# Performance work log

Measured on AMD Instinct MI355X. Metric: run time of the kernel, lower is better.

Reference implementation:

```python
import jax, jax.numpy as jnp
import numpy as np


def setup_inputs() -> dict:
    key = jax.random.key(0)
    ks = jax.random.split(key, 13)
    B, T, C = 256, 80, 512
    H = 512
    NC = 6625
    S = 25
    s = 0.02
    inp = {
        "inputs": jax.random.normal(ks[0], (B, T, C), jnp.float32),
        "targets": jax.random.randint(ks[1], (B, S), 0, NC),
        "batch_max_length": S,
        "i2h_w": jax.random.normal(ks[2], (H, C), jnp.float32) * s,
        "h2h_w": jax.random.normal(ks[3], (H, H), jnp.float32) * s,
        "h2h_b": jax.random.normal(ks[4], (H,), jnp.float32) * s,
        "score_w": jax.random.normal(ks[5], (1, H), jnp.float32) * s,
        "gru_wih": jax.random.normal(ks[6], (3 * H, C + NC), jnp.float32) * s,
        "gru_whh": jax.random.normal(ks[7], (3 * H, H), jnp.float32) * s,
        "gru_bih": jax.random.normal(ks[8], (3 * H,), jnp.float32) * s,
        "gru_bhh": jax.random.normal(ks[9], (3 * H,), jnp.float32) * s,
        "gen_w": jax.random.normal(ks[10], (NC, H), jnp.float32) * s,
        "gen_b": jax.random.normal(ks[11], (NC,), jnp.float32) * s,
    }
    return inp


def reference(inputs, targets, batch_max_length, i2h_w, h2h_w, h2h_b, score_w,
              gru_wih, gru_whh, gru_bih, gru_bhh, gen_w, gen_b):
    B, T, C = inputs.shape
    H = h2h_w.shape[0]
    NC = gen_w.shape[0]
    S = batch_max_length

    # i2h has no bias; same result every step, hoisted out of the loop
    batch_H_proj = inputs @ i2h_w.T  # [B, T, H]
    # teacher-forcing one-hots for all steps: [S, B, NC]
    onehots = jax.nn.one_hot(targets.T, NC, dtype=inputs.dtype)

    def gru_cell(x, h):
        gi = x @ gru_wih.T + gru_bih  # [B, 3H]
        gh = h @ gru_whh.T + gru_bhh  # [B, 3H]
        i_r, i_z, i_n = jnp.split(gi, 3, axis=1)
        h_r, h_z, h_n = jnp.split(gh, 3, axis=1)
        r = jax.nn.sigmoid(i_r + h_r)
        z = jax.nn.sigmoid(i_z + h_z)
        n = jnp.tanh(i_n + r * h_n)
        return (1.0 - z) * n + z * h

    def step(h, onehot_t):
        prev_proj = h @ h2h_w.T + h2h_b  # [B, H]
        res = jnp.tanh(batch_H_proj + prev_proj[:, None, :])  # [B, T, H]
        e = jnp.einsum('bth,h->bt', res, score_w[0])  # [B, T]
        alpha = jax.nn.softmax(e, axis=1)
        context = jnp.einsum('bt,btc->bc', alpha, inputs)  # [B, C]
        x = jnp.concatenate([context, onehot_t], axis=1)  # [B, C+NC]
        h_new = gru_cell(x, h)
        return h_new, h_new

    h0 = jnp.zeros((B, H), inputs.dtype)
    _, hiddens = jax.lax.scan(step, h0, onehots)  # [S, B, H]
    output = jnp.transpose(hiddens, (1, 0, 2))  # [B, S, H]
    probs = output @ gen_w.T + gen_b  # [B, S, NC] (training path: no softmax)
    return probs
```

## Files before the change

kernel.cpp:

```cpp
#include <hip/hip_runtime.h>
#include <stdint.h>

typedef float f32x4 __attribute__((ext_vector_type(4)));
typedef int i32x4 __attribute__((ext_vector_type(4)));

#define LOG2E 1.4426950408889634f

__device__ __forceinline__ float bf2f(unsigned short u) {
  union { unsigned int i; float f; } x; x.i = ((unsigned int)u) << 16; return x.f;
}
__device__ __forceinline__ float bfu_lo(unsigned u) {
  union { unsigned int i; float f; } x; x.i = u << 16; return x.f;
}
__device__ __forceinline__ float bfu_hi(unsigned u) {
  union { unsigned int i; float f; } x; x.i = u & 0xffff0000u; return x.f;
}
__device__ __forceinline__ unsigned short f2bf(float f) {
  union { float f; unsigned int i; } x; x.f = f;
  unsigned int u = x.i + 0x7fffu + ((x.i >> 16) & 1u);
  return (unsigned short)(u >> 16);
}
__device__ __forceinline__ float fexp2(float x) {
#if __has_builtin(__builtin_amdgcn_exp2f)
  return __builtin_amdgcn_exp2f(x);
#else
  return exp2f(x);
#endif
}
__device__ __forceinline__ float frcp(float x) {
#if __has_builtin(__builtin_amdgcn_rcpf)
  return __builtin_amdgcn_rcpf(x);
#else
  return 1.f / x;
#endif
}
__device__ __forceinline__ float fast_exp(float x) { return fexp2(x * LOG2E); }
__device__ __forceinline__ float fast_tanh(float x) {
  float e = fexp2(x * (2.f * LOG2E));
  return 1.f - 2.f * frcp(e + 1.f);
}
__device__ __forceinline__ float fast_sigmoid(float x) {
  return frcp(1.f + fexp2(-x * LOG2E));
}

__device__ __forceinline__ void mfma_bf16_16x16x32(f32x4& d, i32x4 a, i32x4 b) {
  asm("v_mfma_f32_16x16x32_bf16 %0, %1, %2, %0" : "+v"(d) : "v"(a), "v"(b));
}

__device__ __forceinline__ void stage16(const unsigned short* g, unsigned short* lds_wave_base, int lane) {
#if __has_builtin(__builtin_amdgcn_global_load_lds)
  __builtin_amdgcn_global_load_lds(
      (const __attribute__((address_space(1))) unsigned int*)(uintptr_t)g,
      (__attribute__((address_space(3))) unsigned int*)(uintptr_t)lds_wave_base,
      16, 0, 0);
#else
  i32x4 v = *(const i32x4*)g;
  *(i32x4*)(lds_wave_base + lane * 8) = v;
#endif
}

__device__ __forceinline__ void xcd_swizzle(int& bx, int& by) {
  int nx = gridDim.x, nwg = nx * gridDim.y;
  if ((nwg & 7) == 0) {
    int id = by * nx + bx;
    int q = nwg >> 3;
    int swz = (id & 7) * q + (id >> 3);
    bx = swz % nx;
    by = swz / nx;
  }
}

#define BM 128
#define BN 128
#define BK 32

template <bool OUT_BF16, bool BIAS>
__device__ __forceinline__ void gemm_body(
    const unsigned short* __restrict__ A, const unsigned short* __restrict__ B,
    void* __restrict__ Cout, const float* __restrict__ bias,
    int K, int ldc, int nbound, int m0, int n0)
{
  __shared__ __align__(16) unsigned short lA[BM * BK];
  __shared__ __align__(16) unsigned short lB[BN * BK];
  const int tid = threadIdx.x;
  const int lane = tid & 63;
  const int w = tid >> 6;
  const int wm = w >> 1, wn = w & 1;
  const int frag_row = lane & 15;
  const int kgrp = lane >> 4;

  f32x4 acc[4][4];
#pragma unroll
  for (int i = 0; i < 4; ++i)
#pragma unroll
    for (int j = 0; j < 4; ++j) acc[i][j] = 0.f;

  const int nK = K / BK;
  const int c0 = tid, c1 = tid + 256;
  for (int kt = 0; kt < nK; ++kt) {
    const int kb = kt * BK;
    stage16(A + (size_t)(m0 + (c0 >> 2)) * K + kb + (c0 & 3) * 8, lA + (w * 64) * 8, lane);
    stage16(A + (size_t)(m0 + (c1 >> 2)) * K + kb + (c1 & 3) * 8, lA + (256 + w * 64) * 8, lane);
    stage16(B + (size_t)(n0 + (c0 >> 2)) * K + kb + (c0 & 3) * 8, lB + (w * 64) * 8, lane);
    stage16(B + (size_t)(n0 + (c1 >> 2)) * K + kb + (c1 & 3) * 8, lB + (256 + w * 64) * 8, lane);
    __syncthreads();

    i32x4 af[4], bfr[4];
#pragma unroll
    for (int i = 0; i < 4; ++i) {
      int ra = wm * 64 + i * 16 + frag_row;
      af[i] = *(const i32x4*)&lA[ra * BK + kgrp * 8];
      int rb = wn * 64 + i * 16 + frag_row;
      bfr[i] = *(const i32x4*)&lB[rb * BK + kgrp * 8];
    }
#pragma unroll
    for (int i = 0; i < 4; ++i)
#pragma unroll
      for (int j = 0; j < 4; ++j) mfma_bf16_16x16x32(acc[i][j], af[i], bfr[j]);
    __syncthreads();
  }

  const int crow = (lane >> 4) * 4;
  const int ccol = lane & 15;
#pragma unroll
  for (int i = 0; i < 4; ++i) {
#pragma unroll
    for (int j = 0; j < 4; ++j) {
      int gn = n0 + wn * 64 + j * 16 + ccol;
      if (gn < nbound) {
        float bv = BIAS ? bias[gn] : 0.f;
        int gmb = m0 + wm * 64 + i * 16 + crow;
#pragma unroll
        for (int r = 0; r < 4; ++r) {
          float v = acc[i][j][r] + bv;
          if (OUT_BF16) ((unsigned short*)Cout)[(size_t)(gmb + r) * ldc + gn] = f2bf(v);
          else          ((float*)Cout)[(size_t)(gmb + r) * ldc + gn] = v;
        }
      }
    }
  }
}

__global__ __launch_bounds__(256) void gemm_bf16out_kernel(
    const unsigned short* __restrict__ A, const unsigned short* __restrict__ B,
    unsigned short* __restrict__ C, int K, int ldc) {
  int bx = blockIdx.x, by = blockIdx.y;
  xcd_swizzle(bx, by);
  gemm_body<true, false>(A, B, C, nullptr, K, ldc, 1 << 30, by * BM, bx * BN);
}
__global__ __launch_bounds__(256) void gemm_f32bias_kernel(
    const unsigned short* __restrict__ A, const unsigned short* __restrict__ B,
    float* __restrict__ C, const float* __restrict__ bias, int K, int ldc, int nbound) {
  int bx = blockIdx.x, by = blockIdx.y;
  xcd_swizzle(bx, by);
  gemm_body<false, true>(A, B, C, bias, K, ldc, nbound, by * BM, bx * BN);
}

__global__ __launch_bounds__(256) void cast_bf16_kernel(
    const float* __restrict__ src, unsigned short* __restrict__ dst, int n4) {
  int i = blockIdx.x * 256 + threadIdx.x;
  if (i < n4) {
    float4 v = ((const float4*)src)[i];
    ushort4 o;
    o.x = f2bf(v.x); o.y = f2bf(v.y); o.z = f2bf(v.z); o.w = f2bf(v.w);
    ((ushort4*)dst)[i] = o;
  }
}
__global__ __launch_bounds__(256) void cast_wihc_kernel(
    const float* __restrict__ wih, unsigned short* __restrict__ dst) {
  int i = blockIdx.x * 256 + threadIdx.x;
  int j = i >> 9, c = i & 511;
  dst[i] = f2bf(wih[(size_t)j * 7137 + c]);
}
__global__ __launch_bounds__(256) void pack_h2h_kernel(
    const float* __restrict__ src, unsigned short* __restrict__ dst) {
  int i = blockIdx.x * 256 + threadIdx.x;
  int row = i >> 9, c = i & 511;
  int kb = c >> 3, kk = c & 7;
  dst[((size_t)kb * 512 + row) * 8 + kk] = f2bf(src[i]);
}
__global__ __launch_bounds__(256) void cast_genw_kernel(
    const float* __restrict__ g, unsigned short* __restrict__ dst) {
  int i = blockIdx.x * 256 + threadIdx.x;
  if (i < 6656 * 512) {
    int nrow = i >> 9, c = i & 511;
    float v = (nrow < 6625) ? g[(size_t)nrow * 512 + c] : 0.f;
    dst[i] = f2bf(v);
  }
}
__global__ __launch_bounds__(256) void transpose_oh_kernel(
    const float* __restrict__ wih, unsigned short* __restrict__ dst) {
  __shared__ float tile[32][33];
  int t0 = blockIdx.x * 32;
  int j0 = blockIdx.y * 32;
  int c = threadIdx.x & 31;
  int r4 = threadIdx.x >> 5;
#pragma unroll
  for (int rr = 0; rr < 4; ++rr) {
    int r = r4 + rr * 8;
    int tcol = t0 + c;
    tile[r][c] = (tcol < 6625) ? wih[(size_t)(j0 + r) * 7137 + 512 + tcol] : 0.f;
  }
  __syncthreads();
#pragma unroll
  for (int rr = 0; rr < 4; ++rr) {
    int r = r4 + rr * 8;
    int trow = t0 + r;
    if (trow < 6625) dst[(size_t)trow * 1536 + j0 + c] = f2bf(tile[c][r]);
  }
}

__global__ __launch_bounds__(512) void attn_step_kernel(
    const unsigned short* __restrict__ proj_bf,
    const unsigned short* __restrict__ inputs_bf,
    const unsigned short* __restrict__ h2hP,
    const float* __restrict__ h2h_b,
    const float* __restrict__ score_w,
    const unsigned short* __restrict__ h_in,
    unsigned short* __restrict__ ctx_bf,
    int s)
{
  __shared__ float h_lds[512];
  __shared__ float pp_lds[512];
  __shared__ float e_s[80];
  __shared__ float alpha_s[80];

  const int tid = threadIdx.x;
  const int lane = tid & 63;
  const int w = tid >> 6;
  const int b = blockIdx.x;

  if (s > 0) h_lds[tid] = bf2f(h_in[b * 512 + tid]);
  __syncthreads();

  float pacc = h2h_b[tid];
  if (s > 0) {
    const unsigned short* wp = h2hP + (size_t)tid * 8;
#pragma unroll 4
    for (int kb = 0; kb < 64; ++kb) {
      union { i32x4 v; unsigned int u[4]; } wu;
      wu.v = *(const i32x4*)(wp + (size_t)kb * 4096);
#pragma unroll
      for (int q = 0; q < 4; ++q) {
        pacc = fmaf(bfu_lo(wu.u[q]), h_lds[kb * 8 + 2 * q], pacc);
        pacc = fmaf(bfu_hi(wu.u[q]), h_lds[kb * 8 + 2 * q + 1], pacc);
      }
    }
  }
  pp_lds[tid] = pacc;
  __syncthreads();

  float ppv[8], swv[8];
#pragma unroll
  for (int j = 0; j < 8; ++j) ppv[j] = pp_lds[lane * 8 + j];
  *(float4*)&swv[0] = *(const float4*)(score_w + lane * 8);
  *(float4*)&swv[4] = *(const float4*)(score_w + lane * 8 + 4);

  for (int t = w; t < 80; t += 8) {
    union { i32x4 v; unsigned int u[4]; } u;
    u.v = *(const i32x4*)(proj_bf + (size_t)(b * 80 + t) * 512 + lane * 8);
    float acc = 0.f;
#pragma unroll
    for (int q = 0; q < 4; ++q) {
      acc += fast_tanh(bfu_lo(u.u[q]) + ppv[2 * q]) * swv[2 * q];
      acc += fast_tanh(bfu_hi(u.u[q]) + ppv[2 * q + 1]) * swv[2 * q + 1];
    }
#pragma unroll
    for (int m = 32; m >= 1; m >>= 1) acc += __shfl_xor(acc, m, 64);
    if (lane == 0) e_s[t] = acc;
  }
  __syncthreads();
  if (w == 0) {
    float v0 = e_s[lane];
    float v1 = (lane < 16) ? e_s[64 + lane] : -1e30f;
    float mx = fmaxf(v0, v1);
#pragma unroll
    for (int m = 32; m >= 1; m >>= 1) mx = fmaxf(mx, __shfl_xor(mx, m, 64));
    float a0 = fast_exp(v0 - mx);
    float a1 = (lane < 16) ? fast_exp(v1 - mx) : 0.f;
    float sm = a0 + a1;
#pragma unroll
    for (int m = 32; m >= 1; m >>= 1) sm += __shfl_xor(sm, m, 64);
    float inv = frcp(sm);
    alpha_s[lane] = a0 * inv;
    if (lane < 16) alpha_s[64 + lane] = a1 * inv;
  }
  __syncthreads();

  float cacc = 0.f;
  const unsigned short* ip = inputs_bf + (size_t)b * 40960;
#pragma unroll 8
  for (int t = 0; t < 80; ++t)
    cacc = fmaf(alpha_s[t], bf2f(ip[t * 512 + tid]), cacc);
  ctx_bf[(size_t)b * 512 + tid] = f2bf(cacc);
}

__global__ __launch_bounds__(256) void gru_step_kernel(
    const unsigned short* __restrict__ h_in,
    const unsigned short* __restrict__ ctx,
    const unsigned short* __restrict__ whh,
    const unsigned short* __restrict__ wihc,
    const unsigned short* __restrict__ ohT,
    const int* __restrict__ targets,
    const float* __restrict__ bih, const float* __restrict__ bhh,
    unsigned short* __restrict__ h_out,
    unsigned short* __restrict__ hid_bf,
    int s)
{
  __shared__ __align__(16) char sm[49152];
  unsigned short* lAh = (unsigned short*)sm;
  unsigned short* lAc = lAh + 4096;
  unsigned short* lBw = lAh + 8192;
  unsigned short* lBi = lAh + 14336;

  const int tid = threadIdx.x;
  const int lane = tid & 63;
  const int w = tid >> 6;
  const int fr = lane & 15, kg = lane >> 4;
  const int wm = w >> 1, wn = w & 1;
  const int m0 = blockIdx.y * 64;
  const int c0 = blockIdx.x * 32;

  f32x4 ag[2][3], ai[2][3];
#pragma unroll
  for (int i = 0; i < 2; ++i)
#pragma unroll
    for (int j = 0; j < 3; ++j) { ag[i][j] = 0.f; ai[i][j] = 0.f; }

  for (int kt = 0; kt < 8; ++kt) {
    const int kb = kt * 64;
#pragma unroll
    for (int i = 0; i < 2; ++i) {
      int c = tid + i * 256;
      int row = c >> 3, k8 = c & 7;
      int sk8 = k8 ^ (row & 7);
      stage16(h_in + (size_t)(m0 + row) * 512 + kb + sk8 * 8, lAh + (i * 256 + w * 64) * 8, lane);
      stage16(ctx  + (size_t)(m0 + row) * 512 + kb + sk8 * 8, lAc + (i * 256 + w * 64) * 8, lane);
    }
#pragma unroll
    for (int i = 0; i < 3; ++i) {
      int c = tid + i * 256;
      int br = c >> 3, k8 = c & 7;
      int sk8 = k8 ^ (br & 7);
      int gr = (br >> 5) * 512 + c0 + (br & 31);
      stage16(whh  + (size_t)gr * 512 + kb + sk8 * 8, lBw + (i * 256 + w * 64) * 8, lane);
      stage16(wihc + (size_t)gr * 512 + kb + sk8 * 8, lBi + (i * 256 + w * 64) * 8, lane);
    }
    __syncthreads();

#pragma unroll
    for (int ks = 0; ks < 2; ++ks) {
      const int kc = ks * 4 + kg;
      i32x4 ah[2], ac[2], bw[3], bi[3];
#pragma unroll
      for (int i = 0; i < 2; ++i) {
        int r = wm * 32 + i * 16 + fr;
        int off = r * 64 + (kc ^ (r & 7)) * 8;
        ah[i] = *(const i32x4*)&lAh[off];
        ac[i] = *(const i32x4*)&lAc[off];
      }
#pragma unroll
      for (int j = 0; j < 3; ++j) {
        int r = wn * 48 + j * 16 + fr;
        int off = r * 64 + (kc ^ (r & 7)) * 8;
        bw[j] = *(const i32x4*)&lBw[off];
        bi[j] = *(const i32x4*)&lBi[off];
      }
#pragma unroll
      for (int i = 0; i < 2; ++i)
#pragma unroll
        for (int j = 0; j < 3; ++j) {
          mfma_bf16_16x16x32(ag[i][j], ah[i], bw[j]);
          mfma_bf16_16x16x32(ai[i][j], ac[i], bi[j]);
        }
    }
    __syncthreads();
  }

  float* accg = (float*)sm;
  float* acci = accg + 6144;
  const int crow = (lane >> 4) * 4;
  const int ccol = lane & 15;
#pragma unroll
  for (int i = 0; i < 2; ++i)
#pragma unroll
    for (int j = 0; j < 3; ++j) {
      int col = wn * 48 + j * 16 + ccol;
#pragma unroll
      for (int r = 0; r < 4; ++r) {
        int row = wm * 32 + i * 16 + crow + r;
        accg[row * 96 + col] = ag[i][j][r];
        acci[row * 96 + col] = ai[i][j][r];
      }
    }
  __syncthreads();

#pragma unroll
  for (int e = tid; e < 2048; e += 256) {
    int row = e >> 5, cc = e & 31;
    int b = m0 + row, ch = c0 + cc;
    int tgt = targets[b * 25 + s];
    const unsigned short* oh = ohT + (size_t)tgt * 1536;
    float ghr = accg[row * 96 + cc]      + bhh[ch];
    float ghz = accg[row * 96 + 32 + cc] + bhh[512 + ch];
    float ghn = accg[row * 96 + 64 + cc] + bhh[1024 + ch];
    float gir = acci[row * 96 + cc]      + bih[ch]        + bf2f(oh[ch]);
    float giz = acci[row * 96 + 32 + cc] + bih[512 + ch]  + bf2f(oh[512 + ch]);
    float gin = acci[row * 96 + 64 + cc] + bih[1024 + ch] + bf2f(oh[1024 + ch]);
    float r_ = fast_sigmoid(gir + ghr);
    float z_ = fast_sigmoid(giz + ghz);
    float n_ = fast_tanh(gin + r_ * ghn);
    float h = (1.f - z_) * n_ + z_ * bf2f(h_in[(size_t)b * 512 + ch]);
    unsigned short hb = f2bf(h);
    h_out[(size_t)b * 512 + ch] = hb;
    hid_bf[((size_t)b * 25 + s) * 512 + ch] = hb;
  }
}

extern "C" void kernel_launch(void* const* d_in, const int* in_sizes, int n_in,
                              void* d_out, int out_size, void* d_ws, size_t ws_size,
                              hipStream_t stream) {
  (void)in_sizes; (void)n_in; (void)out_size; (void)ws_size;
  const float* inputs  = (const float*)d_in[0];
  const int*   targets = (const int*)d_in[1];
  const float* i2h_w   = (const float*)d_in[3];
  const float* h2h_w   = (const float*)d_in[4];
  const float* h2h_b   = (const float*)d_in[5];
  const float* score_w = (const float*)d_in[6];
  const float* gru_wih = (const float*)d_in[7];
  const float* gru_whh = (const float*)d_in[8];
  const float* gru_bih = (const float*)d_in[9];
  const float* gru_bhh = (const float*)d_in[10];
  const float* gen_w   = (const float*)d_in[11];
  const float* gen_b   = (const float*)d_in[12];
  float* out = (float*)d_out;

  char* ws = (char*)d_ws;
  size_t off = 0;
  auto alloc = [&](size_t bytes) {
    char* p = ws + off;
    off += (bytes + 255) & ~(size_t)255;
    return p;
  };
  unsigned short* inputs_bf = (unsigned short*)alloc(10485760ull * 2);
  unsigned short* proj_bf   = (unsigned short*)alloc(10485760ull * 2);
  unsigned short* i2h_bf    = (unsigned short*)alloc(262144ull * 2);
  unsigned short* h2hP_bf   = (unsigned short*)alloc(262144ull * 2);
  unsigned short* whh_bf    = (unsigned short*)alloc(786432ull * 2);
  unsigned short* wihc_bf   = (unsigned short*)alloc(786432ull * 2);
  unsigned short* ohT_bf    = (unsigned short*)alloc(10176000ull * 2);
  unsigned short* genw_bf   = (unsigned short*)alloc(3407872ull * 2);
  unsigned short* ctx_bf    = (unsigned short*)alloc(131072ull * 2);
  unsigned short* hbuf0     = (unsigned short*)alloc(131072ull * 2);
  unsigned short* hbuf1     = (unsigned short*)alloc(131072ull * 2);
  unsigned short* hid_bf    = (unsigned short*)alloc(3276800ull * 2);

  cast_bf16_kernel<<<10240, 256, 0, stream>>>(inputs, inputs_bf, 2621440);
  cast_bf16_kernel<<<256, 256, 0, stream>>>(i2h_w, i2h_bf, 65536);
  pack_h2h_kernel<<<1024, 256, 0, stream>>>(h2h_w, h2hP_bf);
  cast_bf16_kernel<<<768, 256, 0, stream>>>(gru_whh, whh_bf, 196608);
  cast_wihc_kernel<<<3072, 256, 0, stream>>>(gru_wih, wihc_bf);
  transpose_oh_kernel<<<dim3(208, 48), 256, 0, stream>>>(gru_wih, ohT_bf);
  cast_genw_kernel<<<13312, 256, 0, stream>>>(gen_w, genw_bf);
  gemm_bf16out_kernel<<<dim3(4, 160), 256, 0, stream>>>(inputs_bf, i2h_bf, proj_bf, 512, 512);
  hipMemsetAsync(hbuf0, 0, 131072 * 2, stream);

  unsigned short* hb[2] = {hbuf0, hbuf1};
  for (int s = 0; s < 25; ++s) {
    attn_step_kernel<<<256, 512, 0, stream>>>(
        proj_bf, inputs_bf, h2hP_bf, h2h_b, score_w, hb[s & 1], ctx_bf, s);
    gru_step_kernel<<<dim3(16, 4), 256, 0, stream>>>(
        hb[s & 1], ctx_bf, whh_bf, wihc_bf, ohT_bf, targets,
        gru_bih, gru_bhh, hb[(s + 1) & 1], hid_bf, s);
  }

  gemm_f32bias_kernel<<<dim3(52, 50), 256, 0, stream>>>(hid_bf, genw_bf, out, gen_b, 512, 6625, 6625);
}
```

Measured before the change: 975.4 us.

## Widen GEMM K-tile with XOR-swizzled LDS, generalize XCD swizzle, fuse prep casts

The GEMM K-tile grows from 32 to 64 and LDS staging uses an XOR swizzle on the 16-byte chunk index. This halves the number of barrier-separated K iterations and should cut LDS bank conflicts on fragment reads. The XCD swizzle now also handles grid sizes that are not a multiple of 8, so the 52x50 output GEMM gets remapped too. The seven weight and input cast/pack kernels are merged into one launch to save launch overhead. The cost is more LDS per block, which may lower occupancy.

```diff
diff --git a/kernel.cpp b/kernel.cpp
--- a/kernel.cpp
+++ b/kernel.cpp
@@ -61,18 +61,17 @@
 
 __device__ __forceinline__ void xcd_swizzle(int& bx, int& by) {
   int nx = gridDim.x, nwg = nx * gridDim.y;
-  if ((nwg & 7) == 0) {
-    int id = by * nx + bx;
-    int q = nwg >> 3;
-    int swz = (id & 7) * q + (id >> 3);
-    bx = swz % nx;
-    by = swz / nx;
-  }
+  int id = by * nx + bx;
+  int q = nwg >> 3, r = nwg & 7;
+  int x = id & 7, j = id >> 3;
+  int swz = (x < r ? x * (q + 1) : r * (q + 1) + (x - r) * q) + j;
+  bx = swz % nx;
+  by = swz / nx;
 }
 
 #define BM 128
 #define BN 128
-#define BK 32
+#define BK 64
 
 template <bool OUT_BF16, bool BIAS>
 __device__ __forceinline__ void gemm_body(
@@ -86,8 +85,8 @@
   const int lane = tid & 63;
   const int w = tid >> 6;
   const int wm = w >> 1, wn = w & 1;
-  const int frag_row = lane & 15;
-  const int kgrp = lane >> 4;
+  const int fr = lane & 15;
+  const int kg = lane >> 4;
 
   f32x4 acc[4][4];
 #pragma unroll
@@ -96,27 +95,34 @@
     for (int j = 0; j < 4; ++j) acc[i][j] = 0.f;
 
   const int nK = K / BK;
-  const int c0 = tid, c1 = tid + 256;
   for (int kt = 0; kt < nK; ++kt) {
     const int kb = kt * BK;
-    stage16(A + (size_t)(m0 + (c0 >> 2)) * K + kb + (c0 & 3) * 8, lA + (w * 64) * 8, lane);
-    stage16(A + (size_t)(m0 + (c1 >> 2)) * K + kb + (c1 & 3) * 8, lA + (256 + w * 64) * 8, lane);
-    stage16(B + (size_t)(n0 + (c0 >> 2)) * K + kb + (c0 & 3) * 8, lB + (w * 64) * 8, lane);
-    stage16(B + (size_t)(n0 + (c1 >> 2)) * K + kb + (c1 & 3) * 8, lB + (256 + w * 64) * 8, lane);
+#pragma unroll
+    for (int i = 0; i < 4; ++i) {
+      int c = tid + i * 256;
+      int row = c >> 3, k8 = c & 7;
+      int sk8 = k8 ^ (row & 7);
+      stage16(A + (size_t)(m0 + row) * K + kb + sk8 * 8, lA + (i * 256 + w * 64) * 8, lane);
+      stage16(B + (size_t)(n0 + row) * K + kb + sk8 * 8, lB + (i * 256 + w * 64) * 8, lane);
+    }
     __syncthreads();
 
-    i32x4 af[4], bfr[4];
-#pragma unroll
-    for (int i = 0; i < 4; ++i) {
-      int ra = wm * 64 + i * 16 + frag_row;
-      af[i] = *(const i32x4*)&lA[ra * BK + kgrp * 8];
-      int rb = wn * 64 + i * 16 + frag_row;
-      bfr[i] = *(const i32x4*)&lB[rb * BK + kgrp * 8];
-    }
-#pragma unroll
-    for (int i = 0; i < 4; ++i)
-#pragma unroll
-      for (int j = 0; j < 4; ++j) mfma_bf16_16x16x32(acc[i][j], af[i], bfr[j]);
+#pragma unroll
+    for (int ks = 0; ks < 2; ++ks) {
+      const int kc = ks * 4 + kg;
+      i32x4 af[4], bfr[4];
+#pragma unroll
+      for (int i = 0; i < 4; ++i) {
+        int ra = wm * 64 + i * 16 + fr;
+        af[i] = *(const i32x4*)&lA[ra * 64 + (kc ^ (ra & 7)) * 8];
+        int rb = wn * 64 + i * 16 + fr;
+        bfr[i] = *(const i32x4*)&lB[rb * 64 + (kc ^ (rb & 7)) * 8];
+      }
+#pragma unroll
+      for (int i = 0; i < 4; ++i)
+#pragma unroll
+        for (int j = 0; j < 4; ++j) mfma_bf16_16x16x32(acc[i][j], af[i], bfr[j]);
+    }
     __syncthreads();
   }
 
@@ -156,57 +162,67 @@
   gemm_body<false, true>(A, B, C, bias, K, ldc, nbound, by * BM, bx * BN);
 }
 
-__global__ __launch_bounds__(256) void cast_bf16_kernel(
-    const float* __restrict__ src, unsigned short* __restrict__ dst, int n4) {
-  int i = blockIdx.x * 256 + threadIdx.x;
-  if (i < n4) {
-    float4 v = ((const float4*)src)[i];
-    ushort4 o;
-    o.x = f2bf(v.x); o.y = f2bf(v.y); o.z = f2bf(v.z); o.w = f2bf(v.w);
-    ((ushort4*)dst)[i] = o;
-  }
-}
-__global__ __launch_bounds__(256) void cast_wihc_kernel(
-    const float* __restrict__ wih, unsigned short* __restrict__ dst) {
-  int i = blockIdx.x * 256 + threadIdx.x;
-  int j = i >> 9, c = i & 511;
-  dst[i] = f2bf(wih[(size_t)j * 7137 + c]);
-}
-__global__ __launch_bounds__(256) void pack_h2h_kernel(
-    const float* __restrict__ src, unsigned short* __restrict__ dst) {
-  int i = blockIdx.x * 256 + threadIdx.x;
-  int row = i >> 9, c = i & 511;
-  int kb = c >> 3, kk = c & 7;
-  dst[((size_t)kb * 512 + row) * 8 + kk] = f2bf(src[i]);
-}
-__global__ __launch_bounds__(256) void cast_genw_kernel(
-    const float* __restrict__ g, unsigned short* __restrict__ dst) {
-  int i = blockIdx.x * 256 + threadIdx.x;
-  if (i < 6656 * 512) {
+__global__ __launch_bounds__(256) void prep_kernel(
+    const float* __restrict__ inputs, const float* __restrict__ i2h_w,
+    const float* __restrict__ h2h_w, const float* __restrict__ gru_whh,
+    const float* __restrict__ gru_wih, const float* __restrict__ gen_w,
+    unsigned short* __restrict__ inputs_bf, unsigned short* __restrict__ i2h_bf,
+    unsigned short* __restrict__ h2hP, unsigned short* __restrict__ whh_bf,
+    unsigned short* __restrict__ wihc_bf, unsigned short* __restrict__ genw_bf,
+    unsigned short* __restrict__ ohT_bf)
+{
+  __shared__ float tile[32][33];
+  const int blk = blockIdx.x;
+  const int t = threadIdx.x;
+
+  if (blk < 10240) {
+    int i = blk * 256 + t;
+    float4 v = ((const float4*)inputs)[i];
+    ushort4 o; o.x = f2bf(v.x); o.y = f2bf(v.y); o.z = f2bf(v.z); o.w = f2bf(v.w);
+    ((ushort4*)inputs_bf)[i] = o;
+  } else if (blk < 10496) {
+    int i = (blk - 10240) * 256 + t;
+    float4 v = ((const float4*)i2h_w)[i];
+    ushort4 o; o.x = f2bf(v.x); o.y = f2bf(v.y); o.z = f2bf(v.z); o.w = f2bf(v.w);
+    ((ushort4*)i2h_bf)[i] = o;
+  } else if (blk < 11520) {
+    int i = (blk - 10496) * 256 + t;
+    int row = i >> 9, c = i & 511;
+    int kb = c >> 3, kk = c & 7;
+    h2hP[((size_t)kb * 512 + row) * 8 + kk] = f2bf(h2h_w[i]);
+  } else if (blk < 12288) {
+    int i = (blk - 11520) * 256 + t;
+    float4 v = ((const float4*)gru_whh)[i];
+    ushort4 o; o.x = f2bf(v.x); o.y = f2bf(v.y); o.z = f2bf(v.z); o.w = f2bf(v.w);
+    ((ushort4*)whh_bf)[i] = o;
+  } else if (blk < 15360) {
+    int i = (blk - 12288) * 256 + t;
+    int j = i >> 9, c = i & 511;
+    wihc_bf[i] = f2bf(gru_wih[(size_t)j * 7137 + c]);
+  } else if (blk < 28672) {
+    int i = (blk - 15360) * 256 + t;
     int nrow = i >> 9, c = i & 511;
-    float v = (nrow < 6625) ? g[(size_t)nrow * 512 + c] : 0.f;
-    dst[i] = f2bf(v);
-  }
-}
-__global__ __launch_bounds__(256) void transpose_oh_kernel(
-    const float* __restrict__ wih, unsigned short* __restrict__ dst) {
-  __shared__ float tile[32][33];
-  int t0 = blockIdx.x * 32;
-  int j0 = blockIdx.y * 32;
-  int c = threadIdx.x & 31;
-  int r4 = threadIdx.x >> 5;
-#pragma unroll
-  for (int rr = 0; rr < 4; ++rr) {
-    int r = r4 + rr * 8;
-    int tcol = t0 + c;
-    tile[r][c] = (tcol < 6625) ? wih[(size_t)(j0 + r) * 7137 + 512 + tcol] : 0.f;
-  }
-  __syncthreads();
-#pragma unroll
-  for (int rr = 0; rr < 4; ++rr) {
-    int r = r4 + rr * 8;
-    int trow = t0 + r;
-    if (trow < 6625) dst[(size_t)trow * 1536 + j0 + c] = f2bf(tile[c][r]);
+    float v = (nrow < 6625) ? gen_w[(size_t)nrow * 512 + c] : 0.f;
+    genw_bf[i] = f2bf(v);
+  } else {
+    int tb = blk - 28672;
+    int t0 = (tb % 208) * 32;
+    int j0 = (tb / 208) * 32;
+    int c = t & 31;
+    int r4 = t >> 5;
+#pragma unroll
+    for (int rr = 0; rr < 4; ++rr) {
+      int r = r4 + rr * 8;
+      int tcol = t0 + c;
+      tile[r][c] = (tcol < 6625) ? gru_wih[(size_t)(j0 + r) * 7137 + 512 + tcol] : 0.f;
+    }
+    __syncthreads();
+#pragma unroll
+    for (int rr = 0; rr < 4; ++rr) {
+      int r = r4 + rr * 8;
+      int trow = t0 + r;
+      if (trow < 6625) ohT_bf[(size_t)trow * 1536 + j0 + c] = f2bf(tile[c][r]);
+    }
   }
 }
 
@@ -455,13 +471,9 @@
   unsigned short* hbuf1     = (unsigned short*)alloc(131072ull * 2);
   unsigned short* hid_bf    = (unsigned short*)alloc(3276800ull * 2);
 
-  cast_bf16_kernel<<<10240, 256, 0, stream>>>(inputs, inputs_bf, 2621440);
-  cast_bf16_kernel<<<256, 256, 0, stream>>>(i2h_w, i2h_bf, 65536);
-  pack_h2h_kernel<<<1024, 256, 0, stream>>>(h2h_w, h2hP_bf);
-  cast_bf16_kernel<<<768, 256, 0, stream>>>(gru_whh, whh_bf, 196608);
-  cast_wihc_kernel<<<3072, 256, 0, stream>>>(gru_wih, wihc_bf);
-  transpose_oh_kernel<<<dim3(208, 48), 256, 0, stream>>>(gru_wih, ohT_bf);
-  cast_genw_kernel<<<13312, 256, 0, stream>>>(gen_w, genw_bf);
+  prep_kernel<<<38656, 256, 0, stream>>>(
+      inputs, i2h_w, h2h_w, gru_whh, gru_wih, gen_w,
+      inputs_bf, i2h_bf, h2hP_bf, whh_bf, wihc_bf, genw_bf, ohT_bf);
   gemm_bf16out_kernel<<<dim3(4, 160), 256, 0, stream>>>(inputs_bf, i2h_bf, proj_bf, 512, 512);
   hipMemsetAsync(hbuf0, 0, 131072 * 2, stream);
 
```

Measured after the change: 952.7 us, median of 2. 2.3% less time.
